# Performance work log

Hardware: AMD Instinct MI355X
Metric: run time of the kernel (lower is better)

## Reference

```python
import jax, jax.numpy as jnp
import numpy as np

B, L, D, H, FF = 2, 2048, 1024, 16, 4096
DH = D // H
EPS = 1e-5  # torch LayerNorm default


def _layernorm(x, g, b):
    mu = jnp.mean(x, axis=-1, keepdims=True)
    var = jnp.mean(jnp.square(x - mu), axis=-1, keepdims=True)
    return (x - mu) * jax.lax.rsqrt(var + EPS) * g + b


def setup_inputs() -> dict:
    key = jax.random.key(0)
    ks = jax.random.split(key, 8)
    s = 0.02  # typical init scale for weights
    return {
        "x": jax.random.normal(ks[0], (B, L, D), jnp.float32),
        "pos_embed": jax.random.normal(ks[1], (1, L, D), jnp.float32) * s,
        "ln1_g": jnp.ones((D,), jnp.float32),
        "ln1_b": jnp.zeros((D,), jnp.float32),
        "Wq": jax.random.normal(ks[2], (D, D), jnp.float32) * s,
        "Wk": jax.random.normal(ks[3], (D, D), jnp.float32) * s,
        "Wv": jax.random.normal(ks[4], (D, D), jnp.float32) * s,
        "Wo": jax.random.normal(ks[5], (D, D), jnp.float32) * s,
        "bo": jnp.zeros((D,), jnp.float32),
        "ln2_g": jnp.ones((D,), jnp.float32),
        "ln2_b": jnp.zeros((D,), jnp.float32),
        "W1": jax.random.normal(ks[6], (D, FF), jnp.float32) * s,
        "b1": jnp.zeros((FF,), jnp.float32),
        "W2": jax.random.normal(ks[7], (FF, D), jnp.float32) * s,
        "b2": jnp.zeros((D,), jnp.float32),
    }


def reference(x, pos_embed, ln1_g, ln1_b, Wq, Wk, Wv, Wo, bo, ln2_g, ln2_b, W1, b1, W2, b2):
    scale = DH ** -0.5
    residual = x
    h = _layernorm(x, ln1_g, ln1_b) + pos_embed  # [B,L,D]
    # qkv projections (no bias, qkv_bias=False default), split into heads
    q = (h @ Wq).reshape(B, L, H, DH).transpose(0, 2, 1, 3)  # [B,H,L,DH]
    k = (h @ Wk).reshape(B, L, H, DH).transpose(0, 2, 1, 3)
    v = (h @ Wv).reshape(B, L, H, DH).transpose(0, 2, 1, 3)
    attn = jnp.einsum("bhqd,bhkd->bhqk", q, k) * scale  # [B,H,L,L]
    attn = jax.nn.softmax(attn, axis=-1)
    out = jnp.einsum("bhqk,bhkd->bhqd", attn, v)  # [B,H,L,DH]
    out = out.transpose(0, 2, 1, 3).reshape(B, L, D)
    out = out @ Wo + bo
    x = residual + out
    # MLP with pre-norm
    m = _layernorm(x, ln2_g, ln2_b)
    m = jax.nn.gelu(m @ W1 + b1, approximate=False) @ W2 + b2
    return x + m
```

## Files before the change

kernel.cpp:

```cpp
#include <hip/hip_runtime.h>
#include <hip/hip_bf16.h>
#include <cstdint>

typedef __bf16 bf16_t;
typedef __bf16 bf16x8 __attribute__((ext_vector_type(8)));
typedef __bf16 bf16x4v __attribute__((ext_vector_type(4)));
typedef short s16x4 __attribute__((ext_vector_type(4)));
typedef float f32x4 __attribute__((ext_vector_type(4)));

#define B_ 2
#define L_ 2048
#define D_ 1024
#define H_ 16
#define DH_ 64
#define FF_ 4096
#define M_TOT (B_*L_)

#define CLOG2 0.18033688011112042f


__device__ __forceinline__ void gload_lds16(const void* g, void* l) {
    __builtin_amdgcn_global_load_lds((__attribute__((address_space(1))) void*)g,
                                     (__attribute__((address_space(3))) void*)l,
                                     16, 0, 0);
}

__device__ __forceinline__ float gelu_exact(float v) {
    return 0.5f * v * (1.0f + erff(v * 0.70710678118654752f));
}

__device__ __forceinline__ float fast_exp2(float v) {
    return __builtin_amdgcn_exp2f(v);
}

__global__ void transpose_bf16_kernel(const float* __restrict__ W, bf16_t* __restrict__ WT,
                                      int K, int N) {
    __shared__ float t[32][33];
    int tx = threadIdx.x, ty = threadIdx.y;
    int n0 = blockIdx.x * 32, k0 = blockIdx.y * 32;
#pragma unroll
    for (int i = 0; i < 4; i++)
        t[ty + 8 * i][tx] = W[(size_t)(k0 + ty + 8 * i) * N + n0 + tx];
    __syncthreads();
#pragma unroll
    for (int i = 0; i < 4; i++)
        WT[(size_t)(n0 + ty + 8 * i) * K + k0 + tx] = (bf16_t)t[tx][ty + 8 * i];
}

__global__ __launch_bounds__(256) void ln_kernel(const float* __restrict__ x,
                                                 const float* __restrict__ pos,
                                                 const float* __restrict__ g,
                                                 const float* __restrict__ beta,
                                                 bf16_t* __restrict__ out) {
    int row = blockIdx.x, tid = threadIdx.x;
    const float* xr = x + (size_t)row * D_;
    float v[4];
    float s = 0.f, sq = 0.f;
#pragma unroll
    for (int i = 0; i < 4; i++) {
        float a = xr[tid + 256 * i];
        v[i] = a; s += a; sq += a * a;
    }
#pragma unroll
    for (int o = 32; o > 0; o >>= 1) { s += __shfl_xor(s, o); sq += __shfl_xor(sq, o); }
    __shared__ float red[8];
    int wid = tid >> 6;
    if ((tid & 63) == 0) { red[wid] = s; red[4 + wid] = sq; }
    __syncthreads();
    s  = red[0] + red[1] + red[2] + red[3];
    sq = red[4] + red[5] + red[6] + red[7];
    float mu  = s * (1.f / D_);
    float var = sq * (1.f / D_) - mu * mu;
    float rs  = rsqrtf(var + 1e-5f);
    int l = row & (L_ - 1);
#pragma unroll
    for (int i = 0; i < 4; i++) {
        int c = tid + 256 * i;
        float hv = (v[i] - mu) * rs * g[c] + beta[c];
        if (pos) hv += pos[(size_t)l * D_ + c];
        out[(size_t)row * D_ + c] = (bf16_t)hv;
    }
}

__global__ __launch_bounds__(256) void addbias_kernel(const float* __restrict__ src,
                                                      const float* __restrict__ bias,
                                                      float* __restrict__ dst) {
    int i = (blockIdx.x * 256 + threadIdx.x) * 4;
    float4 v = *(const float4*)(src + i);
    float4 bv = *(const float4*)(bias + (i & (D_ - 1)));
    v.x += bv.x; v.y += bv.y; v.z += bv.z; v.w += bv.w;
    *(float4*)(dst + i) = v;
}

template <int EPI, typename OutT>
__global__ __launch_bounds__(256) void gemm_kernel(const bf16_t* __restrict__ A,
                                                   const bf16_t* __restrict__ BT,
                                                   OutT* __restrict__ C,
                                                   const float* __restrict__ bias,
                                                   bf16_t* __restrict__ Vt,
                                                   int M, int N, int K) {
    __shared__ __align__(16) bf16_t sA[128 * 32];
    __shared__ __align__(16) bf16_t sB[128 * 32];
    int tid = threadIdx.x;
    int lane = tid & 63, w = tid >> 6, wy = w >> 1, wx = w & 1;
    int qm = lane & 15, quad = lane >> 4;
    int row0 = blockIdx.y * 128, col0 = blockIdx.x * 128;
    f32x4 acc[4][4] = {};
    int f0 = tid * 8, f1 = f0 + 2048;
    int ra0 = f0 >> 5, ca0 = f0 & 31, ra1 = f1 >> 5, ca1 = f1 & 31;
    const bf16_t* Ab = A  + (size_t)row0 * K;
    const bf16_t* Bb = BT + (size_t)col0 * K;
    for (int k0 = 0; k0 < K; k0 += 32) {
        gload_lds16(Ab + (size_t)ra0 * K + k0 + ca0, &sA[f0]);
        gload_lds16(Ab + (size_t)ra1 * K + k0 + ca1, &sA[f1]);
        gload_lds16(Bb + (size_t)ra0 * K + k0 + ca0, &sB[f0]);
        gload_lds16(Bb + (size_t)ra1 * K + k0 + ca1, &sB[f1]);
        __syncthreads();
        bf16x8 af[4], bfr[4];
#pragma unroll
        for (int mt = 0; mt < 4; mt++)
            af[mt] = *(const bf16x8*)&sA[(wy * 64 + mt * 16 + qm) * 32 + quad * 8];
#pragma unroll
        for (int nt = 0; nt < 4; nt++)
            bfr[nt] = *(const bf16x8*)&sB[(wx * 64 + nt * 16 + qm) * 32 + quad * 8];
#pragma unroll
        for (int mt = 0; mt < 4; mt++)
#pragma unroll
            for (int nt = 0; nt < 4; nt++)
                acc[mt][nt] = __builtin_amdgcn_mfma_f32_16x16x32_bf16(af[mt], bfr[nt],
                                                                      acc[mt][nt], 0, 0, 0);
        __syncthreads();
    }
    if (EPI == 4 && col0 >= 2048) {
#pragma unroll
        for (int mt = 0; mt < 4; mt++) {
            int row_base = row0 + wy * 64 + mt * 16 + quad * 4;
            int bb = row_base >> 11, key0 = row_base & 2047;
#pragma unroll
            for (int nt = 0; nt < 4; nt++) {
                int vcol = col0 - 2048 + wx * 64 + nt * 16 + qm;
                int hh = vcol >> 6, dd = vcol & 63;
                bf16x4v pk;
#pragma unroll
                for (int r = 0; r < 4; r++) pk[r] = (bf16_t)acc[mt][nt][r];
                *(bf16x4v*)&Vt[(size_t)(((bb << 4) + hh) * 64 + dd) * 2048 + key0] = pk;
            }
        }
        return;
    }
#pragma unroll
    for (int mt = 0; mt < 4; mt++) {
#pragma unroll
        for (int nt = 0; nt < 4; nt++) {
            int col = col0 + wx * 64 + nt * 16 + qm;
#pragma unroll
            for (int r = 0; r < 4; r++) {
                int row = row0 + wy * 64 + mt * 16 + quad * 4 + r;
                float v = acc[mt][nt][r];
                if (EPI == 2) { v += bias[col]; v = gelu_exact(v); }
                if (EPI == 4) C[(size_t)row * 2048 + col] = (OutT)v;
                else          C[(size_t)row * N + col] = (OutT)v;
            }
        }
    }
}

__global__ __launch_bounds__(256) void gemm_splitk_kernel(const bf16_t* __restrict__ A,
                                                          const bf16_t* __restrict__ BT,
                                                          float* __restrict__ C,
                                                          int N, int Ktot, int Ksplit) {
    __shared__ __align__(16) bf16_t sA[128 * 32];
    __shared__ __align__(16) bf16_t sB[128 * 32];
    int tid = threadIdx.x;
    int lane = tid & 63, w = tid >> 6, wy = w >> 1, wx = w & 1;
    int qm = lane & 15, quad = lane >> 4;
    int row0 = blockIdx.y * 128, col0 = blockIdx.x * 128;
    size_t koff = (size_t)blockIdx.z * Ksplit;
    f32x4 acc[4][4] = {};
    int f0 = tid * 8, f1 = f0 + 2048;
    int ra0 = f0 >> 5, ca0 = f0 & 31, ra1 = f1 >> 5, ca1 = f1 & 31;
    const bf16_t* Ab = A  + (size_t)row0 * Ktot + koff;
    const bf16_t* Bb = BT + (size_t)col0 * Ktot + koff;
    for (int k0 = 0; k0 < Ksplit; k0 += 32) {
        gload_lds16(Ab + (size_t)ra0 * Ktot + k0 + ca0, &sA[f0]);
        gload_lds16(Ab + (size_t)ra1 * Ktot + k0 + ca1, &sA[f1]);
        gload_lds16(Bb + (size_t)ra0 * Ktot + k0 + ca0, &sB[f0]);
        gload_lds16(Bb + (size_t)ra1 * Ktot + k0 + ca1, &sB[f1]);
        __syncthreads();
        bf16x8 af[4], bfr[4];
#pragma unroll
        for (int mt = 0; mt < 4; mt++)
            af[mt] = *(const bf16x8*)&sA[(wy * 64 + mt * 16 + qm) * 32 + quad * 8];
#pragma unroll
        for (int nt = 0; nt < 4; nt++)
            bfr[nt] = *(const bf16x8*)&sB[(wx * 64 + nt * 16 + qm) * 32 + quad * 8];
#pragma unroll
        for (int mt = 0; mt < 4; mt++)
#pragma unroll
            for (int nt = 0; nt < 4; nt++)
                acc[mt][nt] = __builtin_amdgcn_mfma_f32_16x16x32_bf16(af[mt], bfr[nt],
                                                                      acc[mt][nt], 0, 0, 0);
        __syncthreads();
    }
#pragma unroll
    for (int mt = 0; mt < 4; mt++) {
#pragma unroll
        for (int nt = 0; nt < 4; nt++) {
            int col = col0 + wx * 64 + nt * 16 + qm;
#pragma unroll
            for (int r = 0; r < 4; r++) {
                int row = row0 + wy * 64 + mt * 16 + quad * 4 + r;
                atomicAdd(&C[(size_t)row * N + col], acc[mt][nt][r]);
            }
        }
    }
}

__global__ __launch_bounds__(256, 3) void attn_kernel(const bf16_t* __restrict__ QK,
                                                      const bf16_t* __restrict__ Vt,
                                                      bf16_t* __restrict__ O) {
    __shared__ __align__(16) bf16_t sK[64 * 72];
    __shared__ __align__(16) bf16_t sV[64 * 72];
    int tid = threadIdx.x, lane = tid & 63, w = tid >> 6;
    int qm = lane & 15, quad = lane >> 4;
    int q0 = blockIdx.x * 128 + w * 32;
    int bh = blockIdx.y, b = bh >> 4, h = bh & 15;

    const bf16_t* Qbase = QK + (size_t)(b * L_) * 2048 + h * 64;
    const bf16_t* Kbase = Qbase + 1024;
    const bf16_t* Vbase = Vt + (size_t)bh * 64 * 2048;

    bf16x8 qf[2][2];
#pragma unroll
    for (int g = 0; g < 2; g++) {
        const bf16_t* qp = Qbase + (size_t)(q0 + g * 16 + qm) * 2048 + quad * 8;
        qf[g][0] = *(const bf16x8*)qp;
        qf[g][1] = *(const bf16x8*)(qp + 32);
    }

    f32x4 o[2][4] = {};
    float m_[2] = {-1e30f, -1e30f};
    float l_[2] = {0.f, 0.f};

    int sr = tid >> 3, sc = (tid & 7) * 8;
    uint4 kr0 = *(const uint4*)(Kbase + (size_t)sr * 2048 + sc);
    uint4 kr1 = *(const uint4*)(Kbase + (size_t)(32 + sr) * 2048 + sc);
    uint4 vr0 = *(const uint4*)(Vbase + (size_t)sr * 2048 + sc);
    uint4 vr1 = *(const uint4*)(Vbase + (size_t)(32 + sr) * 2048 + sc);

    for (int kv0 = 0; kv0 < L_; kv0 += 64) {
        __syncthreads();
        *(uint4*)&sK[sr * 72 + sc] = kr0;
        *(uint4*)&sK[(32 + sr) * 72 + sc] = kr1;
        *(uint4*)&sV[sr * 72 + sc] = vr0;
        *(uint4*)&sV[(32 + sr) * 72 + sc] = vr1;
        __syncthreads();

        int kn = (kv0 + 64) & (L_ - 1);
        kr0 = *(const uint4*)(Kbase + (size_t)(kn + sr) * 2048 + sc);
        kr1 = *(const uint4*)(Kbase + (size_t)(kn + 32 + sr) * 2048 + sc);
        vr0 = *(const uint4*)(Vbase + (size_t)sr * 2048 + kn + sc);
        vr1 = *(const uint4*)(Vbase + (size_t)(32 + sr) * 2048 + kn + sc);

        s16x4 pf[2][4];
#pragma unroll
        for (int g = 0; g < 2; g++) {
            f32x4 s[4] = {};
#pragma unroll
            for (int kt = 0; kt < 4; kt++)
#pragma unroll
                for (int ks = 0; ks < 2; ks++) {
                    bf16x8 kf = *(const bf16x8*)&sK[(kt * 16 + qm) * 72 + ks * 32 + quad * 8];
                    s[kt] = __builtin_amdgcn_mfma_f32_16x16x32_bf16(kf, qf[g][ks], s[kt], 0, 0, 0);
                }
            float mx = s[0][0];
#pragma unroll
            for (int kt = 0; kt < 4; kt++) {
                mx = fmaxf(mx, fmaxf(fmaxf(s[kt][0], s[kt][1]), fmaxf(s[kt][2], s[kt][3])));
            }
            mx = fmaxf(mx, __shfl_xor(mx, 16));
            mx = fmaxf(mx, __shfl_xor(mx, 32));
            float mnew = fmaxf(m_[g], mx);
            float t = mnew * CLOG2;
            float alpha = fast_exp2(fmaf(m_[g], CLOG2, -t));
            m_[g] = mnew;
            float sum = 0.f;
#pragma unroll
            for (int kt = 0; kt < 4; kt++) {
                union { bf16x4v b; s16x4 i; } u;
#pragma unroll
                for (int r = 0; r < 4; r++) {
                    float p = fast_exp2(fmaf(s[kt][r], CLOG2, -t));
                    sum += p;
                    u.b[r] = (bf16_t)p;
                }
                pf[g][kt] = u.i;
            }
            l_[g] = fmaf(l_[g], alpha, sum);
#pragma unroll
            for (int dt = 0; dt < 4; dt++) o[g][dt] *= alpha;
        }

#pragma unroll
        for (int dt = 0; dt < 4; dt++)
#pragma unroll
            for (int kt = 0; kt < 4; kt++) {
                s16x4 vf = *(const s16x4*)&sV[(dt * 16 + qm) * 72 + kt * 16 + quad * 4];
                o[0][dt] = __builtin_amdgcn_mfma_f32_16x16x16bf16_1k(vf, pf[0][kt], o[0][dt], 0, 0, 0);
                o[1][dt] = __builtin_amdgcn_mfma_f32_16x16x16bf16_1k(vf, pf[1][kt], o[1][dt], 0, 0, 0);
            }
    }

#pragma unroll
    for (int g = 0; g < 2; g++) {
        float lt = l_[g];
        lt += __shfl_xor(lt, 16);
        lt += __shfl_xor(lt, 32);
        float rl = 1.0f / lt;
        size_t row = (size_t)(b * L_ + q0 + g * 16 + qm);
#pragma unroll
        for (int dt = 0; dt < 4; dt++) {
            bf16x4v pk;
#pragma unroll
            for (int r = 0; r < 4; r++) pk[r] = (bf16_t)(o[g][dt][r] * rl);
            *(bf16x4v*)&O[row * D_ + h * 64 + dt * 16 + quad * 4] = pk;
        }
    }
}


extern "C" void kernel_launch(void* const* d_in, const int* in_sizes, int n_in,
                              void* d_out, int out_size, void* d_ws, size_t ws_size,
                              hipStream_t stream) {
    const float* x   = (const float*)d_in[0];
    const float* pos = (const float*)d_in[1];
    const float* g1  = (const float*)d_in[2];
    const float* be1 = (const float*)d_in[3];
    const float* Wq  = (const float*)d_in[4];
    const float* Wk  = (const float*)d_in[5];
    const float* Wv  = (const float*)d_in[6];
    const float* Wo  = (const float*)d_in[7];
    const float* bo  = (const float*)d_in[8];
    const float* g2  = (const float*)d_in[9];
    const float* be2 = (const float*)d_in[10];
    const float* W1  = (const float*)d_in[11];
    const float* b1m = (const float*)d_in[12];
    const float* W2  = (const float*)d_in[13];
    const float* b2m = (const float*)d_in[14];

    char* ws = (char*)d_ws;
    const size_t MB = 1ull << 20;
    bf16_t* W2T   = (bf16_t*)(ws + 0);
    float*  x2    = (float*) (ws + 8 * MB);
    bf16_t* ff1   = (bf16_t*)(ws + 24 * MB);
    bf16_t* qk    = (bf16_t*)(ws + 24 * MB);
    bf16_t* Vt    = (bf16_t*)(ws + 40 * MB);
    bf16_t* hb    = (bf16_t*)(ws + 48 * MB);
    bf16_t* attnO = (bf16_t*)(ws + 56 * MB);
    bf16_t* mb    = (bf16_t*)(ws + 56 * MB);
    bf16_t* W1T   = (bf16_t*)(ws + 64 * MB);
    bf16_t* WqkvT = (bf16_t*)(ws + 72 * MB);
    bf16_t* WoT   = (bf16_t*)(ws + 78 * MB);

    dim3 tb(32, 8);
    transpose_bf16_kernel<<<dim3(32, 32), tb, 0, stream>>>(Wq, WqkvT, D_, D_);
    transpose_bf16_kernel<<<dim3(32, 32), tb, 0, stream>>>(Wk, WqkvT + 1024 * 1024, D_, D_);
    transpose_bf16_kernel<<<dim3(32, 32), tb, 0, stream>>>(Wv, WqkvT + 2048 * 1024, D_, D_);
    transpose_bf16_kernel<<<dim3(32, 32), tb, 0, stream>>>(Wo, WoT, D_, D_);
    transpose_bf16_kernel<<<dim3(128, 32), tb, 0, stream>>>(W1, W1T, D_, FF_);
    transpose_bf16_kernel<<<dim3(32, 128), tb, 0, stream>>>(W2, W2T, FF_, D_);

    ln_kernel<<<M_TOT, 256, 0, stream>>>(x, pos, g1, be1, hb);

    gemm_kernel<4, bf16_t><<<dim3(24, 32), 256, 0, stream>>>(hb, WqkvT, qk, nullptr,
                                                             Vt, M_TOT, 3072, D_);

    attn_kernel<<<dim3(16, 32), 256, 0, stream>>>(qk, Vt, attnO);

    addbias_kernel<<<M_TOT * D_ / 1024, 256, 0, stream>>>(x, bo, x2);
    gemm_splitk_kernel<<<dim3(8, 32, 2), 256, 0, stream>>>(attnO, WoT, x2,
                                                           D_, D_, D_ / 2);

    ln_kernel<<<M_TOT, 256, 0, stream>>>(x2, nullptr, g2, be2, mb);

    addbias_kernel<<<M_TOT * D_ / 1024, 256, 0, stream>>>(x2, b2m, (float*)d_out);

    gemm_kernel<2, bf16_t><<<dim3(32, 32), 256, 0, stream>>>(mb, W1T, ff1, b1m,
                                                             nullptr, M_TOT, FF_, D_);

    gemm_splitk_kernel<<<dim3(8, 32, 2), 256, 0, stream>>>(ff1, W2T, (float*)d_out,
                                                           D_, FF_, FF_ / 2);

    (void)in_sizes; (void)n_in; (void)out_size; (void)ws_size;
}
```

Baseline: 454.8 us.

## Swizzle GEMM LDS layout, deepen K tile to 64, merge QKVO transposes

The main GEMM kernel now stages a 128x64 K-slab per iteration instead of 128x32, halving the number of barrier pairs, and XOR-swizzles the LDS column chunks to avoid bank conflicts on the MFMA fragment reads. The split-K GEMM gets the same swizzle at K=32. The four square weight transposes are merged into one launch using blockIdx.z, and the W2 split-K factor goes from 2 to 4 for more parallelism at the cost of more atomic traffic. The larger LDS footprint (32KB) may reduce occupancy.

```diff
diff --git a/kernel.cpp b/kernel.cpp
--- a/kernel.cpp
+++ b/kernel.cpp
@@ -45,6 +45,24 @@
 #pragma unroll
     for (int i = 0; i < 4; i++)
         WT[(size_t)(n0 + ty + 8 * i) * K + k0 + tx] = (bf16_t)t[tx][ty + 8 * i];
+}
+
+__global__ void transpose_qkvo_kernel(const float* __restrict__ Wq, const float* __restrict__ Wk,
+                                      const float* __restrict__ Wv, const float* __restrict__ Wo,
+                                      bf16_t* __restrict__ WqkvT, bf16_t* __restrict__ WoT) {
+    int z = blockIdx.z;
+    const float* W = (z == 0) ? Wq : (z == 1) ? Wk : (z == 2) ? Wv : Wo;
+    bf16_t* dst = (z < 3) ? (WqkvT + (size_t)z * 1024 * 1024) : WoT;
+    __shared__ float t[32][33];
+    int tx = threadIdx.x, ty = threadIdx.y;
+    int n0 = blockIdx.x * 32, k0 = blockIdx.y * 32;
+#pragma unroll
+    for (int i = 0; i < 4; i++)
+        t[ty + 8 * i][tx] = W[(size_t)(k0 + ty + 8 * i) * D_ + n0 + tx];
+    __syncthreads();
+#pragma unroll
+    for (int i = 0; i < 4; i++)
+        dst[(size_t)(n0 + ty + 8 * i) * D_ + k0 + tx] = (bf16_t)t[tx][ty + 8 * i];
 }
 
 __global__ __launch_bounds__(256) void ln_kernel(const float* __restrict__ x,
@@ -99,36 +117,56 @@
                                                    const float* __restrict__ bias,
                                                    bf16_t* __restrict__ Vt,
                                                    int M, int N, int K) {
-    __shared__ __align__(16) bf16_t sA[128 * 32];
-    __shared__ __align__(16) bf16_t sB[128 * 32];
+    __shared__ __align__(16) bf16_t sA[128 * 64];
+    __shared__ __align__(16) bf16_t sB[128 * 64];
     int tid = threadIdx.x;
     int lane = tid & 63, w = tid >> 6, wy = w >> 1, wx = w & 1;
     int qm = lane & 15, quad = lane >> 4;
     int row0 = blockIdx.y * 128, col0 = blockIdx.x * 128;
     f32x4 acc[4][4] = {};
-    int f0 = tid * 8, f1 = f0 + 2048;
-    int ra0 = f0 >> 5, ca0 = f0 & 31, ra1 = f1 >> 5, ca1 = f1 & 31;
+    int sf[4], sra[4], scol[4];
+#pragma unroll
+    for (int c = 0; c < 4; c++) {
+        int f = tid * 8 + c * 2048;
+        sf[c] = f;
+        sra[c] = f >> 6;
+        int ch = (f >> 3) & 7;
+        scol[c] = ((ch ^ (sra[c] & 7)) << 3);
+    }
     const bf16_t* Ab = A  + (size_t)row0 * K;
     const bf16_t* Bb = BT + (size_t)col0 * K;
-    for (int k0 = 0; k0 < K; k0 += 32) {
-        gload_lds16(Ab + (size_t)ra0 * K + k0 + ca0, &sA[f0]);
-        gload_lds16(Ab + (size_t)ra1 * K + k0 + ca1, &sA[f1]);
-        gload_lds16(Bb + (size_t)ra0 * K + k0 + ca0, &sB[f0]);
-        gload_lds16(Bb + (size_t)ra1 * K + k0 + ca1, &sB[f1]);
-        __syncthreads();
-        bf16x8 af[4], bfr[4];
-#pragma unroll
-        for (int mt = 0; mt < 4; mt++)
-            af[mt] = *(const bf16x8*)&sA[(wy * 64 + mt * 16 + qm) * 32 + quad * 8];
-#pragma unroll
-        for (int nt = 0; nt < 4; nt++)
-            bfr[nt] = *(const bf16x8*)&sB[(wx * 64 + nt * 16 + qm) * 32 + quad * 8];
-#pragma unroll
-        for (int mt = 0; mt < 4; mt++)
-#pragma unroll
-            for (int nt = 0; nt < 4; nt++)
-                acc[mt][nt] = __builtin_amdgcn_mfma_f32_16x16x32_bf16(af[mt], bfr[nt],
-                                                                      acc[mt][nt], 0, 0, 0);
+    int aoff[4][2], boff[4][2];
+#pragma unroll
+    for (int t = 0; t < 4; t++)
+#pragma unroll
+        for (int ks = 0; ks < 2; ks++) {
+            int Ra = wy * 64 + t * 16 + qm;
+            int Rb = wx * 64 + t * 16 + qm;
+            int ch = ks * 4 + quad;
+            aoff[t][ks] = Ra * 64 + ((ch ^ (Ra & 7)) << 3);
+            boff[t][ks] = Rb * 64 + ((ch ^ (Rb & 7)) << 3);
+        }
+    for (int k0 = 0; k0 < K; k0 += 64) {
+#pragma unroll
+        for (int c = 0; c < 4; c++) {
+            gload_lds16(Ab + (size_t)sra[c] * K + k0 + scol[c], &sA[sf[c]]);
+            gload_lds16(Bb + (size_t)sra[c] * K + k0 + scol[c], &sB[sf[c]]);
+        }
+        __syncthreads();
+#pragma unroll
+        for (int ks = 0; ks < 2; ks++) {
+            bf16x8 af[4], bfr[4];
+#pragma unroll
+            for (int mt = 0; mt < 4; mt++) af[mt] = *(const bf16x8*)&sA[aoff[mt][ks]];
+#pragma unroll
+            for (int nt = 0; nt < 4; nt++) bfr[nt] = *(const bf16x8*)&sB[boff[nt][ks]];
+#pragma unroll
+            for (int mt = 0; mt < 4; mt++)
+#pragma unroll
+                for (int nt = 0; nt < 4; nt++)
+                    acc[mt][nt] = __builtin_amdgcn_mfma_f32_16x16x32_bf16(af[mt], bfr[nt],
+                                                                          acc[mt][nt], 0, 0, 0);
+        }
         __syncthreads();
     }
     if (EPI == 4 && col0 >= 2048) {
@@ -177,23 +215,37 @@
     int row0 = blockIdx.y * 128, col0 = blockIdx.x * 128;
     size_t koff = (size_t)blockIdx.z * Ksplit;
     f32x4 acc[4][4] = {};
-    int f0 = tid * 8, f1 = f0 + 2048;
-    int ra0 = f0 >> 5, ca0 = f0 & 31, ra1 = f1 >> 5, ca1 = f1 & 31;
+    int sf[2], sra[2], scol[2];
+#pragma unroll
+    for (int c = 0; c < 2; c++) {
+        int f = tid * 8 + c * 2048;
+        sf[c] = f;
+        sra[c] = f >> 5;
+        int ch = (f >> 3) & 3;
+        scol[c] = ((ch ^ (sra[c] & 3)) << 3);
+    }
+    int aoff[4], boff[4];
+#pragma unroll
+    for (int t = 0; t < 4; t++) {
+        int Ra = wy * 64 + t * 16 + qm;
+        int Rb = wx * 64 + t * 16 + qm;
+        aoff[t] = Ra * 32 + ((quad ^ (Ra & 3)) << 3);
+        boff[t] = Rb * 32 + ((quad ^ (Rb & 3)) << 3);
+    }
     const bf16_t* Ab = A  + (size_t)row0 * Ktot + koff;
     const bf16_t* Bb = BT + (size_t)col0 * Ktot + koff;
     for (int k0 = 0; k0 < Ksplit; k0 += 32) {
-        gload_lds16(Ab + (size_t)ra0 * Ktot + k0 + ca0, &sA[f0]);
-        gload_lds16(Ab + (size_t)ra1 * Ktot + k0 + ca1, &sA[f1]);
-        gload_lds16(Bb + (size_t)ra0 * Ktot + k0 + ca0, &sB[f0]);
-        gload_lds16(Bb + (size_t)ra1 * Ktot + k0 + ca1, &sB[f1]);
+#pragma unroll
+        for (int c = 0; c < 2; c++) {
+            gload_lds16(Ab + (size_t)sra[c] * Ktot + k0 + scol[c], &sA[sf[c]]);
+            gload_lds16(Bb + (size_t)sra[c] * Ktot + k0 + scol[c], &sB[sf[c]]);
+        }
         __syncthreads();
         bf16x8 af[4], bfr[4];
 #pragma unroll
-        for (int mt = 0; mt < 4; mt++)
-            af[mt] = *(const bf16x8*)&sA[(wy * 64 + mt * 16 + qm) * 32 + quad * 8];
-#pragma unroll
-        for (int nt = 0; nt < 4; nt++)
-            bfr[nt] = *(const bf16x8*)&sB[(wx * 64 + nt * 16 + qm) * 32 + quad * 8];
+        for (int mt = 0; mt < 4; mt++) af[mt] = *(const bf16x8*)&sA[aoff[mt]];
+#pragma unroll
+        for (int nt = 0; nt < 4; nt++) bfr[nt] = *(const bf16x8*)&sB[boff[nt]];
 #pragma unroll
         for (int mt = 0; mt < 4; mt++)
 #pragma unroll
@@ -363,10 +415,7 @@
     bf16_t* WoT   = (bf16_t*)(ws + 78 * MB);
 
     dim3 tb(32, 8);
-    transpose_bf16_kernel<<<dim3(32, 32), tb, 0, stream>>>(Wq, WqkvT, D_, D_);
-    transpose_bf16_kernel<<<dim3(32, 32), tb, 0, stream>>>(Wk, WqkvT + 1024 * 1024, D_, D_);
-    transpose_bf16_kernel<<<dim3(32, 32), tb, 0, stream>>>(Wv, WqkvT + 2048 * 1024, D_, D_);
-    transpose_bf16_kernel<<<dim3(32, 32), tb, 0, stream>>>(Wo, WoT, D_, D_);
+    transpose_qkvo_kernel<<<dim3(32, 32, 4), tb, 0, stream>>>(Wq, Wk, Wv, Wo, WqkvT, WoT);
     transpose_bf16_kernel<<<dim3(128, 32), tb, 0, stream>>>(W1, W1T, D_, FF_);
     transpose_bf16_kernel<<<dim3(32, 128), tb, 0, stream>>>(W2, W2T, FF_, D_);
 
@@ -388,8 +437,8 @@
     gemm_kernel<2, bf16_t><<<dim3(32, 32), 256, 0, stream>>>(mb, W1T, ff1, b1m,
                                                              nullptr, M_TOT, FF_, D_);
 
-    gemm_splitk_kernel<<<dim3(8, 32, 2), 256, 0, stream>>>(ff1, W2T, (float*)d_out,
-                                                           D_, FF_, FF_ / 2);
+    gemm_splitk_kernel<<<dim3(8, 32, 4), 256, 0, stream>>>(ff1, W2T, (float*)d_out,
+                                                           D_, FF_, FF_ / 4);
 
     (void)in_sizes; (void)n_in; (void)out_size; (void)ws_size;
 }
```

New measurement: 449.7 us. Within noise of the previous version (-1.1%).
